# Kernel tuning notes

Hardware: AMD Instinct MI355X
Metric: run time of the kernel (lower is better)

The kernel has to match this reference:

```python
import jax, jax.numpy as jnp
import numpy as np

K = 3      # kernel_size
P = 1      # padding
NS = 2     # new_size = int(ratio*stride) = 2*1
GC = 16    # group_channels
G = 16     # groups = channels // group_channels
C = G * GC # 256
EPS = 1e-5


def _unfold(x):
    # torch.nn.Unfold(K, 1, P, 1): [B,C,H,W] -> [B,C,K,K,Ho,Wo], channel-major (C, kh, kw)
    B, Cc, H, W = x.shape
    xp = jnp.pad(x, ((0, 0), (0, 0), (P, P), (P, P)))
    rows = [jnp.stack([xp[:, :, i:i + H, j:j + W] for j in range(K)], axis=3)
            for i in range(K)]
    return jnp.stack(rows, axis=2)  # [B,C,K,K,H,W]


def _conv1x1(x, w, b=None):
    y = jnp.einsum('bihw,oi->bohw', x, w)
    if b is not None:
        y = y + b[None, :, None, None]
    return y


def reference(x, w1, bn_gamma, bn_beta, bn_mean, bn_var, w2, b2, w3, b3):
    B, Cc, H, W = x.shape
    xu = _unfold(x).reshape(B, G, GC, K, K, H, W)
    # three max-pooled descriptors
    x1 = jnp.max(xu.reshape(B, G, 4, GC // 4, K, K, H, W), axis=2).reshape(B, -1, H, W)
    x2 = jnp.max(xu, axis=3).reshape(B, -1, H, W)  # max over kh
    x3 = jnp.max(xu, axis=4).reshape(B, -1, H, W)  # max over kw
    w = jnp.concatenate([x1, x2, x3], axis=1)      # [B, G*(gc//4*K*K + 2*gc*K), H, W]
    # conv1 (1x1, no bias) + BN + ReLU
    w = _conv1x1(w, w1)
    inv = bn_gamma / jnp.sqrt(bn_var + EPS)
    w = w * inv[None, :, None, None] + (bn_beta - bn_mean * inv)[None, :, None, None]
    w = jax.nn.relu(w)
    # separable dynamic kernel: outer product over (kh,ns) x (kw,ns)
    wa = _conv1x1(w, w2, b2).reshape(B, G, 1, K, 1, NS, 1, H, W)
    wb = _conv1x1(w, w3, b3).reshape(B, G, 1, 1, K, 1, NS, H, W)
    wt = (wa * wb).reshape(B, G, 1, K * K, NS, NS, H, W)
    wt = jax.nn.softmax(wt, axis=3)
    # apply dynamic kernel: broadcast multiply, mean over K*K
    xv = xu.reshape(B, G, GC, K * K, 1, 1, H, W)
    out = jnp.mean(xv * wt, axis=3)                 # [B,G,GC,NS,NS,H,W]
    out = out.reshape(B, C, NS, NS, H, W)
    out = out.transpose(0, 1, 4, 2, 5, 3)           # [B,C,H,NS,W,NS]
    return out.reshape(B, C, H * NS, W * NS)


def setup_inputs() -> dict:
    key = jax.random.key(0)
    ks = jax.random.split(key, 6)
    in1 = G * (K * GC * 2 + K * K * (GC // 4))   # 2112
    out1 = G * NS * K                             # 96
    x = jax.random.normal(ks[0], (4, C, 56, 56), dtype=jnp.float32)
    w1 = jax.random.normal(ks[1], (out1, in1), dtype=jnp.float32) * 0.02
    w2 = jax.random.normal(ks[2], (out1, out1), dtype=jnp.float32) * 0.1
    b2 = jax.random.normal(ks[3], (out1,), dtype=jnp.float32) * 0.02
    w3 = jax.random.normal(ks[4], (out1, out1), dtype=jnp.float32) * 0.1
    b3 = jax.random.normal(ks[5], (out1,), dtype=jnp.float32) * 0.02
    return {
        'x': x, 'w1': w1,
        'bn_gamma': jnp.ones((out1,), jnp.float32),
        'bn_beta': jnp.zeros((out1,), jnp.float32),
        'bn_mean': jnp.zeros((out1,), jnp.float32),
        'bn_var': jnp.ones((out1,), jnp.float32),
        'w2': w2, 'b2': b2, 'w3': w3, 'b3': b3,
    }
```

## Files before the change

kernel.cpp:

```cpp
#include <hip/hip_runtime.h>

typedef __attribute__((ext_vector_type(8))) _Float16 half8;
typedef __attribute__((ext_vector_type(4))) _Float16 half4;
typedef __attribute__((ext_vector_type(4))) float floatx4;

__device__ inline void gld16(const _Float16* g, _Float16* lds) {
  __builtin_amdgcn_global_load_lds(
      (const __attribute__((address_space(1))) unsigned int*)g,
      (__attribute__((address_space(3))) unsigned int*)lds, 16, 0, 0);
}

__global__ __launch_bounds__(256) void kDescC(const float* __restrict__ x,
                                              const float* __restrict__ w1,
                                              const float* __restrict__ w2,
                                              const float* __restrict__ w3,
                                              _Float16* __restrict__ descF,
                                              _Float16* __restrict__ w1f,
                                              _Float16* __restrict__ w2f,
                                              _Float16* __restrict__ w3f) {
  const int bid = blockIdx.x;
  const int t = threadIdx.x;

  if (bid >= 3584) {
    int i = (bid - 3584) * 256 + t;
    if (i < 202752) w1f[i] = (_Float16)w1[i];
    else if (i < 211968) w2f[i - 202752] = (_Float16)w2[i - 202752];
    else if (i < 221184) w3f[i - 211968] = (_Float16)w3[i - 211968];
    return;
  }

  int g = bid & 15;
  int h = (bid >> 4) % 56;
  int b = bid / 896;

  __shared__ __align__(16) _Float16 xb[144 * 72];
  __shared__ __align__(16) int tOf[132][4];

  if (t < 132) {
    int dl = t;
    int r0, r1, r2, r3;
    if (dl < 36) {
      int a3 = dl / 9, rem = dl % 9, k1 = rem / 3, k2 = rem % 3;
      int br = (k2 * 3 + k1) * 16 + a3;
      r0 = br; r1 = br + 4; r2 = br + 8; r3 = br + 12;
    } else if (dl < 84) {
      int u = dl - 36, gc = u / 3, k2 = u % 3;
      r0 = (k2 * 3 + 0) * 16 + gc;
      r1 = (k2 * 3 + 1) * 16 + gc;
      r2 = (k2 * 3 + 2) * 16 + gc;
      r3 = r0;
    } else {
      int u = dl - 84, gc = u / 3, k1 = u % 3;
      r0 = (0 + k1) * 16 + gc;
      r1 = (3 + k1) * 16 + gc;
      r2 = (6 + k1) * 16 + gc;
      r3 = r0;
    }
    tOf[dl][0] = r0 * 144 + ((r0 >> 4) & 7);
    tOf[dl][1] = r1 * 144 + ((r1 >> 4) & 7);
    tOf[dl][2] = r2 * 144 + ((r2 >> 4) & 7);
    tOf[dl][3] = r3 * 144 + ((r3 >> 4) & 7);
  }

  {
    const long xp = ((long)b * 256 + g * 16) * 3136;
#pragma unroll
    for (int i = 0; i < 7; ++i) {
      int idx = t + i * 256;
      if (idx < 1728) {
        int r = (idx * 2731) >> 15;
        int c4 = idx - r * 12 + 1;
        int kk = r >> 4, ch = r & 15;
        int k2 = (kk >= 6) ? 2 : (kk >= 3 ? 1 : 0);
        int k1 = kk - 3 * k2;
        int t2 = k2 * 56 + h;
        int q3 = (t2 * 683) >> 11;
        int s = t2 - q3 * 3;
        int gr = q3 + k1 - 1;
        int grc = min(max(gr, 0), 55);
        const float* rp = x + xp + (long)ch * 3136 + (long)grc * 56 + (s - 1) + c4 * 4;
        float fv[4];
        __builtin_memcpy(fv, rp, 16);
        bool rok = (unsigned)gr < 56u;
        half4 hv;
        hv[0] = (_Float16)(rok ? fv[0] : 0.f);
        hv[1] = (_Float16)(rok ? fv[1] : 0.f);
        hv[2] = (_Float16)(rok ? fv[2] : 0.f);
        hv[3] = (_Float16)(rok ? fv[3] : 0.f);
        int chunk = (c4 >> 1) ^ (kk & 7);
        *(half4*)((char*)xb + r * 144 + chunk * 16 + (c4 & 1) * 8) = hv;
      }
    }
#pragma unroll
    for (int i = 0; i < 2; ++i) {
      int idx = t + i * 256;
      if (idx < 288) {
        int r = idx >> 1;
        int c4 = (idx & 1) ? 13 : 0;
        int kk = r >> 4, ch = r & 15;
        int k2 = (kk >= 6) ? 2 : (kk >= 3 ? 1 : 0);
        int k1 = kk - 3 * k2;
        int t2 = k2 * 56 + h;
        int q3 = (t2 * 683) >> 11;
        int s = t2 - q3 * 3;
        int gr = q3 + k1 - 1;
        int grc = min(max(gr, 0), 55);
        bool rok = (unsigned)gr < 56u;
        const float* rp = x + xp + (long)ch * 3136 + (long)grc * 56;
        half4 hv;
#pragma unroll
        for (int e = 0; e < 4; ++e) {
          int cg = c4 * 4 + e + s - 1;
          int cgc = min(max(cg, 0), 55);
          float v = rp[cgc];
          hv[e] = (_Float16)((rok & ((unsigned)cg < 56u)) ? v : 0.f);
        }
        int chunk = (c4 >> 1) ^ (kk & 7);
        *(half4*)((char*)xb + r * 144 + chunk * 16 + (c4 & 1) * 8) = hv;
      }
    }
  }
  __syncthreads();

  const long m00 = ((long)(b * 56 + h)) * 56;
  if (t < 231) {
    int pc = t / 33, dlc = t - pc * 33;
    int dl0 = dlc * 4;
    half8 r8s[4];
    const char* xbb = (const char*)xb;
#pragma unroll
    for (int i = 0; i < 4; ++i) {
      const int4 of = *(const int4*)tOf[dl0 + i];
      half8 v0 = *(const half8*)(xbb + (of.x & ~15) + ((pc ^ (of.x & 15)) << 4));
      half8 v1 = *(const half8*)(xbb + (of.y & ~15) + ((pc ^ (of.y & 15)) << 4));
      half8 v2 = *(const half8*)(xbb + (of.z & ~15) + ((pc ^ (of.z & 15)) << 4));
      half8 v3 = *(const half8*)(xbb + (of.w & ~15) + ((pc ^ (of.w & 15)) << 4));
      half8 a = __builtin_elementwise_max(v0, v1);
      half8 c = __builtin_elementwise_max(v2, v3);
      r8s[i] = __builtin_elementwise_max(a, c);
    }
    int dg0 = (dlc < 9)  ? (g * 36 + dl0)
            : (dlc < 21) ? (576 + g * 48 + (dl0 - 36))
                         : (1344 + g * 48 + (dl0 - 84));
    _Float16* dp = descF + (m00 + pc * 8) * 2112 + dg0;
#pragma unroll
    for (int e = 0; e < 8; ++e) {
      half4 o;
      o[0] = r8s[0][e]; o[1] = r8s[1][e]; o[2] = r8s[2][e]; o[3] = r8s[3][e];
      *(half4*)(dp + (long)e * 2112) = o;
    }
  }
}

__global__ __launch_bounds__(256) void kGemm1(
    const _Float16* __restrict__ descF, const _Float16* __restrict__ w1f,
    _Float16* __restrict__ pacc) {
  __shared__ _Float16 Ab[2][64 * 32];
  __shared__ _Float16 Bb[2][96 * 32];
  const int t = threadIdx.x;
  const int wv = t >> 6, lane = t & 63, quad = lane >> 4, lr = lane & 15;
  const int mt = blockIdx.x / 6, ck = blockIdx.x % 6;
  const long mblk = (long)mt * 64;

  const long agbase = (mblk + (t >> 2)) * 2112 + ck * 352 + (t & 3) * 8;
  const long bg0 = (long)(t >> 2) * 2112 + ck * 352 + (t & 3) * 8;
  const long bg1 = (long)((256 + t) >> 2) * 2112 + ck * 352 + (t & 3) * 8;
  const int wslot = (t >> 6) * 512;

  floatx4 acc[6];
#pragma unroll
  for (int j = 0; j < 6; ++j) acc[j] = {0.f, 0.f, 0.f, 0.f};

  gld16(descF + agbase, &Ab[0][wslot]);
  gld16(w1f + bg0, &Bb[0][wslot]);
  if (t < 128) gld16(w1f + bg1, &Bb[0][2048 + wslot]);

  int buf = 0;
  for (int kt = 0; kt < 11; ++kt) {
    __syncthreads();
    if (kt < 10) {
      int off = (kt + 1) * 32;
      gld16(descF + agbase + off, &Ab[buf ^ 1][wslot]);
      gld16(w1f + bg0 + off, &Bb[buf ^ 1][wslot]);
      if (t < 128) gld16(w1f + bg1 + off, &Bb[buf ^ 1][2048 + wslot]);
    }
    half8 af = *(const half8*)(&Ab[buf][(wv * 16 + lr) * 32 + quad * 8]);
#pragma unroll
    for (int j = 0; j < 6; ++j) {
      half8 bf = *(const half8*)(&Bb[buf][(j * 16 + lr) * 32 + quad * 8]);
      acc[j] = __builtin_amdgcn_mfma_f32_16x16x32_f16(af, bf, acc[j], 0, 0, 0);
    }
    buf ^= 1;
  }

  _Float16* pp = pacc + (long)(ck * 196 + mt) * 6144;
#pragma unroll
  for (int j = 0; j < 6; ++j)
#pragma unroll
    for (int r = 0; r < 4; ++r)
      pp[(wv * 16 + quad * 4 + r) * 96 + j * 16 + lr] = (_Float16)acc[j][r];
}

__global__ __launch_bounds__(256) void kGemm2(
    const _Float16* __restrict__ pacc,
    const float* __restrict__ gamma, const float* __restrict__ beta,
    const float* __restrict__ mean, const float* __restrict__ var,
    const _Float16* __restrict__ w2f, const _Float16* __restrict__ w3f,
    const float* __restrict__ b2, const float* __restrict__ b3,
    _Float16* __restrict__ wtg) {
  __shared__ __align__(16) char smem[24576];
  _Float16* ytF = (_Float16*)smem;
  float* wal = (float*)smem;
  float* wbl = wal + 3072;
  __shared__ float invv[96], biasv[96];

  const int t = threadIdx.x;
  const int wv = t >> 6, lane = t & 63, quad = lane >> 4, lr = lane & 15;
  const int wr = wv & 1, wc = wv >> 1;
  const long mblk = (long)blockIdx.x * 32;

  if (t < 96) {
    float iv = gamma[t] * rsqrtf(var[t] + 1e-5f);
    invv[t] = iv; biasv[t] = beta[t] - mean[t] * iv;
  }
  __syncthreads();

#pragma unroll
  for (int i = 0; i < 3; ++i) {
    int q = t + i * 256;
    int m = q / 24, nq = (q - m * 24) * 4;
    long gbase = (mblk + m) * 96 + nq;
    float s0 = 0.f, s1 = 0.f, s2 = 0.f, s3 = 0.f;
#pragma unroll
    for (int ck = 0; ck < 6; ++ck) {
      half4 v = *(const half4*)(pacc + (long)ck * 1204224 + gbase);
      s0 += (float)v.x; s1 += (float)v.y; s2 += (float)v.z; s3 += (float)v.w;
    }
    half4 o;
    o.x = (_Float16)fmaxf(s0 * invv[nq + 0] + biasv[nq + 0], 0.f);
    o.y = (_Float16)fmaxf(s1 * invv[nq + 1] + biasv[nq + 1], 0.f);
    o.z = (_Float16)fmaxf(s2 * invv[nq + 2] + biasv[nq + 2], 0.f);
    o.w = (_Float16)fmaxf(s3 * invv[nq + 3] + biasv[nq + 3], 0.f);
    *(half4*)(ytF + m * 104 + nq) = o;
  }
  __syncthreads();

  floatx4 aa[3], ab[3];
#pragma unroll
  for (int j = 0; j < 3; ++j) { aa[j] = {0.f,0.f,0.f,0.f}; ab[j] = {0.f,0.f,0.f,0.f}; }
#pragma unroll
  for (int ks = 0; ks < 3; ++ks) {
    half8 af = *(const half8*)(ytF + (wr * 16 + lr) * 104 + ks * 32 + quad * 8);
#pragma unroll
    for (int j = 0; j < 3; ++j) {
      int n = (wc * 3 + j) * 16 + lr;
      int wo = n * 96 + ks * 32 + quad * 8;
      half8 b2v = *(const half8*)(w2f + wo);
      half8 b3v = *(const half8*)(w3f + wo);
      aa[j] = __builtin_amdgcn_mfma_f32_16x16x32_f16(af, b2v, aa[j], 0, 0, 0);
      ab[j] = __builtin_amdgcn_mfma_f32_16x16x32_f16(af, b3v, ab[j], 0, 0, 0);
    }
  }
  __syncthreads();

#pragma unroll
  for (int j = 0; j < 3; ++j) {
    int n = (wc * 3 + j) * 16 + lr;
    float bb2 = b2[n], bb3 = b3[n];
#pragma unroll
    for (int r = 0; r < 4; ++r) {
      int m = wr * 16 + quad * 4 + r;
      wal[m * 96 + n] = aa[j][r] + bb2;
      wbl[m * 96 + n] = ab[j][r] + bb3;
    }
  }
  __syncthreads();

#pragma unroll
  for (int it = 0; it < 8; ++it) {
    int u = t + it * 256;
    int m = u >> 6, rest = u & 63;
    int g = rest >> 2, ns = rest & 3;
    int ns1 = ns >> 1, ns2 = ns & 1;
    float la[3], lb[3];
#pragma unroll
    for (int k = 0; k < 3; ++k) {
      la[k] = wal[m * 96 + (g * 3 + k) * 2 + ns1];
      lb[k] = wbl[m * 96 + (g * 3 + k) * 2 + ns2];
    }
    float lg[9], mx = -1e30f;
#pragma unroll
    for (int k1 = 0; k1 < 3; ++k1)
#pragma unroll
      for (int k2 = 0; k2 < 3; ++k2) {
        float v = la[k1] * lb[k2];
        lg[k1 * 3 + k2] = v;
        mx = v > mx ? v : mx;
      }
    float s = 0.f;
#pragma unroll
    for (int k = 0; k < 9; ++k) { lg[k] = __expf(lg[k] - mx); s += lg[k]; }
    float sc = 1.f / (9.f * s);
    _Float16* dst = wtg + (mblk + m) * 576 + g * 36 + ns * 9;
#pragma unroll
    for (int k = 0; k < 9; ++k) dst[k] = (_Float16)(lg[k] * sc);
  }
}

__global__ __launch_bounds__(256) void kApply(const float* __restrict__ x,
                                              const _Float16* __restrict__ wt,
                                              float* __restrict__ out) {
  int bid = blockIdx.x;
  int g = bid & 15;
  int wh = (bid >> 4) & 1;
  int h = (bid >> 5) % 56;
  int b = bid / 1792;
  int wbase = wh * 28, cbase = g * 16;

  __shared__ _Float16 xr[9 * 16 * 30];
  __shared__ __align__(16) float wtb[28 * 36];
  __shared__ float ob[32 * 57];

  int t = threadIdx.x;

  {
    int wc = t & 31;
    int r0 = t >> 5;
    int wr = wbase + wc - 1;
    int wrc = min(max(wr, 0), 55);
    bool cok = (wc < 30) & ((unsigned)wr < 56u);
    const long xb0 = ((long)b * 256 + cbase) * 3136;
    float vals[18];
#pragma unroll
    for (int i = 0; i < 18; ++i) {
      int row = r0 + i * 8;
      int kk = row >> 4, cl = row & 15;
      int k2 = (kk >= 6) ? 2 : (kk >= 3 ? 1 : 0);
      int k1 = kk - 3 * k2;
      int t2 = k2 * 56 + h;
      int q3 = (t2 * 683) >> 11;
      int gr = q3 + k1 - 1;
      int grc = min(max(gr, 0), 55);
      float v = x[xb0 + (long)cl * 3136 + (long)grc * 56 + wrc];
      vals[i] = (cok & ((unsigned)gr < 56u)) ? v : 0.f;
    }
#pragma unroll
    for (int i = 0; i < 18; ++i) {
      int row = r0 + i * 8;
      if (wc < 30) xr[row * 30 + wc] = (_Float16)vals[i];
    }
  }
  {
    long m0 = ((long)(b * 56 + h)) * 56 + wbase;
    if (t < 252) {
      int p = t / 9, j = t - p * 9;
      half4 v = *(const half4*)(wt + (m0 + p) * 576 + g * 36 + j * 4);
#pragma unroll
      for (int e = 0; e < 4; ++e) {
        int u = j * 4 + e;
        int ns = (u * 57) >> 9;
        int kk = u - ns * 9;
        wtb[p * 36 + kk * 4 + ns] = (float)v[e];
      }
    }
  }
  __syncthreads();

  {
    int j2r[3];
#pragma unroll
    for (int k2 = 0; k2 < 3; ++k2) j2r[k2] = (k2 * 56 + h) % 3;
#pragma unroll
    for (int i = 0; i < 2; ++i) {
      int idx = i * 256 + t;
      int cl = idx & 15;
      int p = idx >> 4;
      if (p < 28) {
        float a0 = 0.f, a1 = 0.f, a2 = 0.f, a3 = 0.f;
#pragma unroll
        for (int k1 = 0; k1 < 3; ++k1)
#pragma unroll
          for (int k2 = 0; k2 < 3; ++k2) {
            float xv = (float)xr[(k2 * 3 + k1) * 480 + cl * 30 + p + j2r[k2]];
            float4 wv = *(const float4*)&wtb[p * 36 + (k1 * 3 + k2) * 4];
            a0 += xv * wv.x; a1 += xv * wv.y; a2 += xv * wv.z; a3 += xv * wv.w;
          }
        int ob0 = cl * 114 + p * 2;
        ob[ob0] = a0;
        ob[ob0 + 1] = a1;
        ob[ob0 + 57] = a2;
        ob[ob0 + 58] = a3;
      }
    }
  }
  __syncthreads();

  {
    int wo = t & 63;
    int r0 = t >> 6;
    const long obase = (((long)b * 256 + cbase) * 112 + 2 * h) * 112 + wh * 56;
#pragma unroll
    for (int i = 0; i < 8; ++i) {
      int row = r0 + i * 4;
      if (wo < 56) {
        int cli = row >> 1, n1 = row & 1;
        out[obase + cli * 12544 + n1 * 112 + wo] = ob[row * 57 + wo];
      }
    }
  }
}

extern "C" void kernel_launch(void* const* d_in, const int* in_sizes, int n_in,
                              void* d_out, int out_size, void* d_ws, size_t ws_size,
                              hipStream_t stream) {
  const float* x = (const float*)d_in[0];
  const float* w1 = (const float*)d_in[1];
  const float* gamma = (const float*)d_in[2];
  const float* beta = (const float*)d_in[3];
  const float* mean = (const float*)d_in[4];
  const float* var = (const float*)d_in[5];
  const float* w2 = (const float*)d_in[6];
  const float* b2 = (const float*)d_in[7];
  const float* w3 = (const float*)d_in[8];
  const float* b3 = (const float*)d_in[9];
  float* out = (float*)d_out;

  _Float16* w1f = (_Float16*)d_ws;
  _Float16* w2f = w1f + 202752;
  _Float16* w3f = w2f + 9216;
  _Float16* wtg = (_Float16*)((char*)d_ws + 442368);
  _Float16* descF = (_Float16*)((char*)d_ws + 14893056);
  _Float16* pacc = (_Float16*)((char*)d_ws + 67878912);

  hipLaunchKernelGGL(kDescC, dim3(4448), dim3(256), 0, stream,
                     x, w1, w2, w3, descF, w1f, w2f, w3f);
  hipLaunchKernelGGL(kGemm1, dim3(1176), dim3(256), 0, stream, descF, w1f, pacc);
  hipLaunchKernelGGL(kGemm2, dim3(392), dim3(256), 0, stream,
                     pacc, gamma, beta, mean, var, w2f, w3f, b2, b3, wtg);
  hipLaunchKernelGGL(kApply, dim3(7168), dim3(256), 0, stream, x, wtg, out);
}
```

Baseline: 152.1 us.

## Process full image rows per block in kApply with vectorized loads and stores

kApply now covers a whole 56-wide output row per block instead of half a row, halving the grid. Each block still stages 9x16 shifted x rows in LDS, but now through 16-byte float4 global loads converted to half4. Only the edge columns fall back to scalar loads. The shift offset is folded into the staged layout, so compute indexing drops the per-k2 column offset, and output is written as float2 stores. The cost is larger LDS use per block and fewer blocks, which may lower occupancy. Load redundancy at the half-row seams goes away.

```diff
diff --git a/kernel.cpp b/kernel.cpp
--- a/kernel.cpp
+++ b/kernel.cpp
@@ -312,100 +312,126 @@
                                               float* __restrict__ out) {
   int bid = blockIdx.x;
   int g = bid & 15;
-  int wh = (bid >> 4) & 1;
-  int h = (bid >> 5) % 56;
-  int b = bid / 1792;
-  int wbase = wh * 28, cbase = g * 16;
-
-  __shared__ _Float16 xr[9 * 16 * 30];
-  __shared__ __align__(16) float wtb[28 * 36];
-  __shared__ float ob[32 * 57];
+  int h = (bid >> 4) % 56;
+  int b = bid / 896;
+  int cbase = g * 16;
+
+  __shared__ __align__(16) _Float16 xr[9 * 16 * 60];
+  __shared__ __align__(16) float wtb[56 * 36];
+  __shared__ float ob[32 * 114];
 
   int t = threadIdx.x;
 
   {
-    int wc = t & 31;
-    int r0 = t >> 5;
-    int wr = wbase + wc - 1;
-    int wrc = min(max(wr, 0), 55);
-    bool cok = (wc < 30) & ((unsigned)wr < 56u);
-    const long xb0 = ((long)b * 256 + cbase) * 3136;
-    float vals[18];
-#pragma unroll
-    for (int i = 0; i < 18; ++i) {
-      int row = r0 + i * 8;
-      int kk = row >> 4, cl = row & 15;
-      int k2 = (kk >= 6) ? 2 : (kk >= 3 ? 1 : 0);
-      int k1 = kk - 3 * k2;
-      int t2 = k2 * 56 + h;
-      int q3 = (t2 * 683) >> 11;
-      int gr = q3 + k1 - 1;
-      int grc = min(max(gr, 0), 55);
-      float v = x[xb0 + (long)cl * 3136 + (long)grc * 56 + wrc];
-      vals[i] = (cok & ((unsigned)gr < 56u)) ? v : 0.f;
-    }
-#pragma unroll
-    for (int i = 0; i < 18; ++i) {
-      int row = r0 + i * 8;
-      if (wc < 30) xr[row * 30 + wc] = (_Float16)vals[i];
-    }
-  }
+    const long xp = ((long)b * 256 + cbase) * 3136;
+#pragma unroll
+    for (int i = 0; i < 7; ++i) {
+      int idx = t + i * 256;
+      if (idx < 1728) {
+        int r = (idx * 2731) >> 15;
+        int c4 = idx - r * 12 + 1;
+        int kk = r >> 4, cl = r & 15;
+        int k2 = (kk >= 6) ? 2 : (kk >= 3 ? 1 : 0);
+        int k1 = kk - 3 * k2;
+        int t2 = k2 * 56 + h;
+        int q3 = (t2 * 683) >> 11;
+        int s = t2 - q3 * 3;
+        int gr = q3 + k1 - 1;
+        int grc = min(max(gr, 0), 55);
+        const float* rp = x + xp + (long)cl * 3136 + (long)grc * 56 + (s - 1) + c4 * 4;
+        float fv[4];
+        __builtin_memcpy(fv, rp, 16);
+        bool rok = (unsigned)gr < 56u;
+        half4 hv;
+        hv[0] = (_Float16)(rok ? fv[0] : 0.f);
+        hv[1] = (_Float16)(rok ? fv[1] : 0.f);
+        hv[2] = (_Float16)(rok ? fv[2] : 0.f);
+        hv[3] = (_Float16)(rok ? fv[3] : 0.f);
+        *(half4*)((char*)xr + r * 120 + c4 * 8) = hv;
+      }
+    }
+#pragma unroll
+    for (int i = 0; i < 2; ++i) {
+      int idx = t + i * 256;
+      if (idx < 288) {
+        int r = idx >> 1;
+        int c4 = (idx & 1) ? 13 : 0;
+        int kk = r >> 4, cl = r & 15;
+        int k2 = (kk >= 6) ? 2 : (kk >= 3 ? 1 : 0);
+        int k1 = kk - 3 * k2;
+        int t2 = k2 * 56 + h;
+        int q3 = (t2 * 683) >> 11;
+        int s = t2 - q3 * 3;
+        int gr = q3 + k1 - 1;
+        int grc = min(max(gr, 0), 55);
+        bool rok = (unsigned)gr < 56u;
+        const float* rp = x + xp + (long)cl * 3136 + (long)grc * 56;
+        half4 hv;
+#pragma unroll
+        for (int e = 0; e < 4; ++e) {
+          int cg = c4 * 4 + e + s - 1;
+          int cgc = min(max(cg, 0), 55);
+          float v = rp[cgc];
+          hv[e] = (_Float16)((rok & ((unsigned)cg < 56u)) ? v : 0.f);
+        }
+        *(half4*)((char*)xr + r * 120 + c4 * 8) = hv;
+      }
+    }
+  }
+
   {
-    long m0 = ((long)(b * 56 + h)) * 56 + wbase;
-    if (t < 252) {
-      int p = t / 9, j = t - p * 9;
-      half4 v = *(const half4*)(wt + (m0 + p) * 576 + g * 36 + j * 4);
-#pragma unroll
-      for (int e = 0; e < 4; ++e) {
-        int u = j * 4 + e;
-        int ns = (u * 57) >> 9;
-        int kk = u - ns * 9;
-        wtb[p * 36 + kk * 4 + ns] = (float)v[e];
-      }
-    }
-  }
-  __syncthreads();
-
-  {
-    int j2r[3];
-#pragma unroll
-    for (int k2 = 0; k2 < 3; ++k2) j2r[k2] = (k2 * 56 + h) % 3;
+    long m0 = ((long)(b * 56 + h)) * 56;
 #pragma unroll
     for (int i = 0; i < 2; ++i) {
-      int idx = i * 256 + t;
+      int idx = t + i * 256;
+      if (idx < 504) {
+        int p = idx / 9, j = idx - p * 9;
+        half4 v = *(const half4*)(wt + (m0 + p) * 576 + g * 36 + j * 4);
+#pragma unroll
+        for (int e = 0; e < 4; ++e) {
+          int u = j * 4 + e;
+          int ns = (u * 57) >> 9;
+          int kk = u - ns * 9;
+          wtb[p * 36 + kk * 4 + ns] = (float)v[e];
+        }
+      }
+    }
+  }
+  __syncthreads();
+
+#pragma unroll
+  for (int i = 0; i < 4; ++i) {
+    int idx = i * 256 + t;
+    if (idx < 896) {
       int cl = idx & 15;
       int p = idx >> 4;
-      if (p < 28) {
-        float a0 = 0.f, a1 = 0.f, a2 = 0.f, a3 = 0.f;
-#pragma unroll
-        for (int k1 = 0; k1 < 3; ++k1)
-#pragma unroll
-          for (int k2 = 0; k2 < 3; ++k2) {
-            float xv = (float)xr[(k2 * 3 + k1) * 480 + cl * 30 + p + j2r[k2]];
-            float4 wv = *(const float4*)&wtb[p * 36 + (k1 * 3 + k2) * 4];
-            a0 += xv * wv.x; a1 += xv * wv.y; a2 += xv * wv.z; a3 += xv * wv.w;
-          }
-        int ob0 = cl * 114 + p * 2;
-        ob[ob0] = a0;
-        ob[ob0 + 1] = a1;
-        ob[ob0 + 57] = a2;
-        ob[ob0 + 58] = a3;
-      }
+      float a0 = 0.f, a1 = 0.f, a2 = 0.f, a3 = 0.f;
+#pragma unroll
+      for (int k1 = 0; k1 < 3; ++k1)
+#pragma unroll
+        for (int k2 = 0; k2 < 3; ++k2) {
+          float xv = (float)xr[((k2 * 3 + k1) * 16 + cl) * 60 + p];
+          float4 wv = *(const float4*)&wtb[p * 36 + (k1 * 3 + k2) * 4];
+          a0 += xv * wv.x; a1 += xv * wv.y; a2 += xv * wv.z; a3 += xv * wv.w;
+        }
+      int ob0 = cl * 228 + p * 2;
+      ob[ob0] = a0;
+      ob[ob0 + 1] = a1;
+      ob[ob0 + 114] = a2;
+      ob[ob0 + 115] = a3;
     }
   }
   __syncthreads();
 
   {
-    int wo = t & 63;
-    int r0 = t >> 6;
-    const long obase = (((long)b * 256 + cbase) * 112 + 2 * h) * 112 + wh * 56;
-#pragma unroll
-    for (int i = 0; i < 8; ++i) {
-      int row = r0 + i * 4;
-      if (wo < 56) {
-        int cli = row >> 1, n1 = row & 1;
-        out[obase + cli * 12544 + n1 * 112 + wo] = ob[row * 57 + wo];
-      }
+    const long obase = (((long)b * 256 + cbase) * 112 + 2 * h) * 112;
+#pragma unroll
+    for (int i = 0; i < 7; ++i) {
+      int u = t + i * 256;
+      int row = u / 56, wo2 = u - row * 56;
+      int cli = row >> 1, n1 = row & 1;
+      float2 v = *(const float2*)&ob[row * 114 + wo2 * 2];
+      *(float2*)&out[obase + cli * 12544 + n1 * 112 + wo2 * 2] = v;
     }
   }
 }
@@ -437,5 +463,5 @@
   hipLaunchKernelGGL(kGemm1, dim3(1176), dim3(256), 0, stream, descF, w1f, pacc);
   hipLaunchKernelGGL(kGemm2, dim3(392), dim3(256), 0, stream,
                      pacc, gamma, beta, mean, var, w2f, w3f, b2, b3, wtg);
-  hipLaunchKernelGGL(kApply, dim3(7168), dim3(256), 0, stream, x, wtg, out);
-}
+  hipLaunchKernelGGL(kApply, dim3(3584), dim3(256), 0, stream, x, wtg, out);
+}
```

Result: slower. 160.0 us (+5.2%).
